# Performance work log

Measured on AMD Instinct MI355X. Metric: run time of the kernel, lower is better.

## Reference

```python
import jax, jax.numpy as jnp
import numpy as np

C = 256      # channels
G = 8        # groups
Cg = C // G  # channels per group (32, %16==0)
KS = 3       # kernel_size
PAD = 1
STRIDE = 1
DIL = 1
OS = 1.0     # offset_scale
DW = 3       # dw_kernel_size
Kg = KS * KS                      # sample points per group (remove_center=0)
D_OM = int(np.ceil(G * Kg * 3 / 8) * 8)  # 216, offset_mask linear out dim
N, H, W = 16, 56, 56


def setup_inputs() -> dict:
    key = jax.random.key(0)
    ks = jax.random.split(key, 8)
    inp = {}
    inp['ref'] = jax.random.normal(ks[0], (N, C, H, W), jnp.float32)
    inp['input'] = jax.random.normal(ks[1], (N, C, H, W), jnp.float32)
    inp['value_w'] = jax.random.normal(ks[2], (C, C), jnp.float32) * (1.0 / np.sqrt(C))
    inp['value_b'] = jnp.zeros((C,), jnp.float32)
    inp['dw_w'] = jax.random.normal(ks[3], (C, 2, DW, DW), jnp.float32) * 0.1
    inp['dw_b'] = jnp.zeros((C,), jnp.float32)
    # original zero-inits offset_mask; use small random weights so sampling is non-trivial
    inp['om_w'] = jax.random.normal(ks[4], (D_OM, C), jnp.float32) * 0.02
    inp['om_b'] = jnp.zeros((D_OM,), jnp.float32)
    inp['out_w'] = jax.random.normal(ks[5], (C, C), jnp.float32) * (1.0 / np.sqrt(C))
    inp['out_b'] = jnp.zeros((C,), jnp.float32)
    return inp


def _dcnv4(ref, inp, value_w, value_b, dw_w, dw_b, om_w, om_b, out_w, out_b):
    n, _, h, w = inp.shape
    # value projection on tokens (N, HW, C)
    tokens = inp.reshape(n, C, h * w).transpose(0, 2, 1)
    xv = (tokens @ value_w.T + value_b).reshape(n, h, w, G, Cg)
    # grouped depthwise-style conv on concat([input, ref]) -> offset/mask features
    cat = jnp.concatenate([inp, ref], axis=1)  # (N, 2C, H, W)
    dw = jax.lax.conv_general_dilated(
        cat, dw_w, (1, 1), ((DW // 2, DW // 2), (DW // 2, DW // 2)),
        dimension_numbers=('NCHW', 'OIHW', 'NCHW'), feature_group_count=C)
    dw = dw + dw_b[None, :, None, None]
    om = dw.transpose(0, 2, 3, 1) @ om_w.T + om_b            # (N,H,W,D_OM)
    om = om[..., :G * Kg * 3].reshape(n, h, w, G, Kg * 3)    # drop pad cols (none here)
    off = om[..., :2 * Kg].reshape(n, h, w, G, Kg, 2)        # (dx, dy) per point
    mask = om[..., 2 * Kg:]                                  # (N,H,W,G,Kg), DCNv4: no softmax
    # sampling locations (index coords): h*stride - pad + i*dil + os*dy
    ii, jj = jnp.meshgrid(jnp.arange(KS), jnp.arange(KS), indexing='ij')
    gy = (ii.reshape(-1) * DIL - PAD).astype(inp.dtype)      # (Kg,)
    gx = (jj.reshape(-1) * DIL - PAD).astype(inp.dtype)
    hh = (jnp.arange(h, dtype=inp.dtype) * STRIDE)[None, :, None, None, None]
    ww = (jnp.arange(w, dtype=inp.dtype) * STRIDE)[None, None, :, None, None]
    iy = hh + gy + OS * off[..., 1]                          # (N,H,W,G,Kg)
    ix = ww + gx + OS * off[..., 0]
    # bilinear sample with zero padding, mask-weighted sum over points
    y0 = jnp.floor(iy); x0 = jnp.floor(ix)
    fy = iy - y0; fx = ix - x0
    y0i = y0.astype(jnp.int32); x0i = x0.astype(jnp.int32)
    nidx = jnp.arange(n)[:, None, None, None, None]
    gidx = jnp.arange(G)[None, None, None, :, None]
    out = jnp.zeros((n, h, w, G, Cg), inp.dtype)
    for dy in (0, 1):
        for dx in (0, 1):
            yy = y0i + dy; xx = x0i + dx
            wgt = (fy if dy else 1.0 - fy) * (fx if dx else 1.0 - fx)
            valid = (yy >= 0) & (yy < h) & (xx >= 0) & (xx < w)
            yyc = jnp.clip(yy, 0, h - 1); xxc = jnp.clip(xx, 0, w - 1)
            gathered = xv[nidx, yyc, xxc, gidx]              # (N,H,W,G,Kg,Cg)
            out = out + jnp.einsum('nhwgp,nhwgpc->nhwgc', wgt * valid * mask, gathered)
    y = out.reshape(n, h * w, C) @ out_w.T + out_b
    return y.transpose(0, 2, 1).reshape(n, C, h, w)


def reference(ref, input, value_w, value_b, dw_w, dw_b, om_w, om_b, out_w, out_b):
    return _dcnv4(ref, input, value_w, value_b, dw_w, dw_b, om_w, om_b, out_w, out_b)
```

## Files before the change

kernel.cpp:

```cpp
#include <hip/hip_runtime.h>

#define HW 3136
#define WID 56
#define HEI 56
#define NCH 256
#define NB 16

typedef __attribute__((ext_vector_type(8))) short bf16x8;
typedef __attribute__((ext_vector_type(8))) unsigned short u16x8;
typedef __attribute__((ext_vector_type(4))) float f32x4;

__device__ __forceinline__ unsigned int f2bf(float f) {
    unsigned int x = __float_as_uint(f);
    return (x + 0x7fffu + ((x >> 16) & 1u)) >> 16;
}
__device__ __forceinline__ float bf2f(unsigned short u) {
    return __uint_as_float(((unsigned int)u) << 16);
}

__global__ __launch_bounds__(256) void cvt_weights(const float* __restrict__ vw,
                                                   const float* __restrict__ ow,
                                                   const float* __restrict__ outw,
                                                   unsigned short* __restrict__ dvw,
                                                   unsigned short* __restrict__ dow,
                                                   unsigned short* __restrict__ doutw) {
    int i = blockIdx.x * 256 + threadIdx.x;
    if (i < 65536) dvw[i] = (unsigned short)f2bf(vw[i]);
    else if (i < 120832) dow[i - 65536] = (unsigned short)f2bf(ow[i - 65536]);
    else if (i < 186368) doutw[i - 120832] = (unsigned short)f2bf(outw[i - 120832]);
}

template <int DOUT, int A_MODE, int OUT_MODE>
__global__ __launch_bounds__(256) void gemm_kernel(const void* __restrict__ Aptr,
                                                   const unsigned short* __restrict__ Bw,
                                                   const float* __restrict__ bias,
                                                   void* __restrict__ Out) {
    int bid = blockIdx.x;
    int nt = bid & 1;
    int mt = (bid >> 1) % 49;
    int n = (bid >> 1) / 49;
    int p0 = mt * 64;
    int tid = threadIdx.x;
    int lane = tid & 63;
    int wv = tid >> 6;
    int wm = wv & 1, wn = wv >> 1;
    int n0 = nt * 128;

    __shared__ __align__(16) char lds[8192 + 16384];
    char* As = lds;
    char* Bs = lds + 8192;

    int l15 = lane & 15;
    int l4 = lane >> 4;

    f32x4 acc[2][4];
    #pragma unroll
    for (int nf = 0; nf < 4; ++nf) {
        int ch = n0 + wn * 64 + nf * 16 + l15;
        float bv = (ch < DOUT) ? bias[ch] : 0.f;
        #pragma unroll
        for (int mf = 0; mf < 2; ++mf) acc[mf][nf] = (f32x4){bv, bv, bv, bv};
    }

    for (int t = 0; t < 4; ++t) {
        int k0 = t * 64;
        if (A_MODE == 0) {
            int px = tid & 63, kq = tid >> 6;
            const float* src = (const float*)Aptr + ((size_t)(n * 256 + k0 + kq * 16)) * HW + p0 + px;
            #pragma unroll
            for (int h = 0; h < 2; ++h) {
                u16x8 v;
                #pragma unroll
                for (int j = 0; j < 8; ++j) v[j] = (unsigned short)f2bf(src[(size_t)(h * 8 + j) * HW]);
                int byte = (px * 128 + (kq * 16 + h * 8) * 2) ^ ((px & 7) << 4);
                *(u16x8*)(As + byte) = v;
            }
        } else if (A_MODE == 1) {
            int px = tid & 63, kq = tid >> 6;
            const unsigned short* src = (const unsigned short*)Aptr + ((size_t)(n * 256 + k0 + kq * 16)) * HW + p0 + px;
            #pragma unroll
            for (int h = 0; h < 2; ++h) {
                u16x8 v;
                #pragma unroll
                for (int j = 0; j < 8; ++j) v[j] = src[(size_t)(h * 8 + j) * HW];
                int byte = (px * 128 + (kq * 16 + h * 8) * 2) ^ ((px & 7) << 4);
                *(u16x8*)(As + byte) = v;
            }
        } else {
            int row = tid >> 2, q = tid & 3;
            const unsigned short* src = (const unsigned short*)Aptr + ((size_t)(n * HW) + p0 + row) * 256 + k0 + q * 16;
            #pragma unroll
            for (int h = 0; h < 2; ++h) {
                u16x8 v = *(const u16x8*)(src + h * 8);
                int byte = (row * 128 + (q * 16 + h * 8) * 2) ^ ((row & 7) << 4);
                *(u16x8*)(As + byte) = v;
            }
        }
        {
            int bch = tid >> 1, kh = tid & 1;
            int ch = n0 + bch;
            bool valid = (ch < DOUT);
            const unsigned short* src = Bw + (size_t)ch * 256 + k0 + kh * 32;
            #pragma unroll
            for (int q = 0; q < 4; ++q) {
                u16x8 v = (u16x8){0, 0, 0, 0, 0, 0, 0, 0};
                if (valid) v = *(const u16x8*)(src + q * 8);
                int byte = (bch * 128 + (kh * 32 + q * 8) * 2) ^ ((bch & 7) << 4);
                *(u16x8*)(Bs + byte) = v;
            }
        }
        __syncthreads();
        bf16x8 af[2][2], bfr[4][2];
        #pragma unroll
        for (int mf = 0; mf < 2; ++mf)
            #pragma unroll
            for (int kf = 0; kf < 2; ++kf) {
                int row = wm * 32 + mf * 16 + l15;
                int byte = (row * 128 + (kf * 32 + l4 * 8) * 2) ^ ((row & 7) << 4);
                af[mf][kf] = *(bf16x8*)(As + byte);
            }
        #pragma unroll
        for (int nf = 0; nf < 4; ++nf)
            #pragma unroll
            for (int kf = 0; kf < 2; ++kf) {
                int row = wn * 64 + nf * 16 + l15;
                int byte = (row * 128 + (kf * 32 + l4 * 8) * 2) ^ ((row & 7) << 4);
                bfr[nf][kf] = *(bf16x8*)(Bs + byte);
            }
        #pragma unroll
        for (int mf = 0; mf < 2; ++mf)
            #pragma unroll
            for (int nf = 0; nf < 4; ++nf)
                #pragma unroll
                for (int kf = 0; kf < 2; ++kf)
                    acc[mf][nf] = __builtin_amdgcn_mfma_f32_16x16x32_bf16(af[mf][kf], bfr[nf][kf], acc[mf][nf], 0, 0, 0);
        __syncthreads();
    }

    #pragma unroll
    for (int mf = 0; mf < 2; ++mf) {
        int pxb = p0 + wm * 32 + mf * 16 + l4 * 4;
        #pragma unroll
        for (int nf = 0; nf < 4; ++nf) {
            int ch = n0 + wn * 64 + nf * 16 + l15;
            if (OUT_MODE == 0) {
                if (ch < DOUT) {
                    float* o = (float*)Out + ((size_t)n * HW + pxb) * DOUT + ch;
                    #pragma unroll
                    for (int j = 0; j < 4; ++j) o[(size_t)j * DOUT] = acc[mf][nf][j];
                }
            } else if (OUT_MODE == 1) {
                unsigned short* o = (unsigned short*)Out + ((size_t)n * HW + pxb) * 256 + ch;
                #pragma unroll
                for (int j = 0; j < 4; ++j) o[(size_t)j * 256] = (unsigned short)f2bf(acc[mf][nf][j]);
            } else {
                float* o = (float*)Out + ((size_t)(n * 256 + ch)) * HW + pxb;
                *(f32x4*)o = acc[mf][nf];
            }
        }
    }
}

__global__ __launch_bounds__(256) void dwconv_kernel(const float* __restrict__ input,
                                                     const float* __restrict__ ref,
                                                     const float* __restrict__ dw_w,
                                                     const float* __restrict__ dw_b,
                                                     unsigned short* __restrict__ out) {
    int blk = blockIdx.x;
    int yt = blk % 14;
    int cb = (blk / 14) & 63;
    int n = blk / (14 * 64);
    int tid = threadIdx.x;
    int x = tid & 63;
    int c = cb * 4 + (tid >> 6);
    int y0 = yt * 4;

    const float* src = (c < 128) ? input : ref;
    int ch0 = (c < 128) ? (2 * c) : (2 * c - 256);

    float w[18];
    #pragma unroll
    for (int i = 0; i < 18; ++i) w[i] = dw_w[c * 18 + i];

    if (x < WID) {
        float bv = dw_b[c];
        float acc[4] = {bv, bv, bv, bv};
        #pragma unroll
        for (int ch = 0; ch < 2; ++ch) {
            const float* base = src + (size_t)(n * NCH + ch0 + ch) * HW;
            #pragma unroll
            for (int r = 0; r < 6; ++r) {
                int yy = y0 - 1 + r;
                bool vy = (yy >= 0) && (yy < HEI);
                const float* row = base + yy * WID;
                float lt = (vy && x > 0) ? row[x - 1] : 0.f;
                float md = vy ? row[x] : 0.f;
                float rt = (vy && x < WID - 1) ? row[x + 1] : 0.f;
                #pragma unroll
                for (int o = 0; o < 4; ++o) {
                    int ky = r - o;
                    if (ky >= 0 && ky < 3) {
                        acc[o] += lt * w[ch * 9 + ky * 3 + 0] + md * w[ch * 9 + ky * 3 + 1] + rt * w[ch * 9 + ky * 3 + 2];
                    }
                }
            }
        }
        unsigned short* o = out + (size_t)(n * NCH + c) * HW + y0 * WID + x;
        #pragma unroll
        for (int j = 0; j < 4; ++j) o[j * WID] = (unsigned short)f2bf(acc[j]);
    }
}

__global__ __launch_bounds__(256) void sample_kernel(const unsigned short* __restrict__ xv,
                                                     const float* __restrict__ om,
                                                     unsigned short* __restrict__ sout) {
    int blk = blockIdx.x;
    int n = blk / (HW / 16);
    int p0 = (blk % (HW / 16)) * 16;
    int tid = threadIdx.x;

    __shared__ __align__(16) float swt[1152][4];
    __shared__ __align__(8) ushort soff[1152][4];

    for (int i = tid; i < 1152; i += 256) {
        int pix = i / 72;
        int r = i % 72;
        int g = r / 9;
        int pt = r % 9;
        int glob = p0 + pix;
        int py = glob / WID, px = glob % WID;
        const float* ob = om + ((size_t)n * HW + glob) * 216 + g * 27;
        float ox = ob[2 * pt];
        float oy = ob[2 * pt + 1];
        float m = ob[18 + pt];
        float iy = (float)(py + pt / 3 - 1) + oy;
        float ix = (float)(px + pt % 3 - 1) + ox;
        float fy0 = floorf(iy), fx0 = floorf(ix);
        float fy = iy - fy0, fx = ix - fx0;
        int y0 = (int)fy0, x0 = (int)fx0;
        #pragma unroll
        for (int dy = 0; dy < 2; ++dy) {
            #pragma unroll
            for (int dx = 0; dx < 2; ++dx) {
                int yy = y0 + dy, xx = x0 + dx;
                bool valid = (yy >= 0) & (yy < HEI) & (xx >= 0) & (xx < WID);
                int yc = min(max(yy, 0), HEI - 1);
                int xc = min(max(xx, 0), WID - 1);
                float wv = (dy ? fy : 1.f - fy) * (dx ? fx : 1.f - fx) * m;
                swt[i][dy * 2 + dx] = valid ? wv : 0.f;
                soff[i][dy * 2 + dx] = (ushort)(yc * WID + xc);
            }
        }
    }
    __syncthreads();

    int pix = tid >> 4;
    int t16 = tid & 15;
    const unsigned short* xvb = xv + (size_t)n * HW * 256;
    unsigned short* so = sout + ((size_t)n * HW + p0 + pix) * 256;

    #pragma unroll
    for (int i = 0; i < 2; ++i) {
        int chunk = t16 + 16 * i;
        int g = chunk >> 2, c8 = chunk & 3;
        int widx = pix * 72 + g * 9;
        const unsigned short* xc = xvb + g * 32 + c8 * 8;
        float acc[8];
        #pragma unroll
        for (int j = 0; j < 8; ++j) acc[j] = 0.f;
        #pragma unroll
        for (int pt = 0; pt < 9; ++pt) {
            float4 w = *(const float4*)&swt[widx + pt][0];
            ushort4 o = *(const ushort4*)&soff[widx + pt][0];
            u16x8 r0 = *(const u16x8*)(xc + (size_t)o.x * 256);
            u16x8 r1 = *(const u16x8*)(xc + (size_t)o.y * 256);
            u16x8 r2 = *(const u16x8*)(xc + (size_t)o.z * 256);
            u16x8 r3 = *(const u16x8*)(xc + (size_t)o.w * 256);
            #pragma unroll
            for (int j = 0; j < 8; ++j) {
                acc[j] += w.x * bf2f(r0[j]) + w.y * bf2f(r1[j]) + w.z * bf2f(r2[j]) + w.w * bf2f(r3[j]);
            }
        }
        u16x8 st;
        #pragma unroll
        for (int j = 0; j < 8; ++j) st[j] = (unsigned short)f2bf(acc[j]);
        *(u16x8*)(so + g * 32 + c8 * 8) = st;
    }
}

extern "C" void kernel_launch(void* const* d_in, const int* in_sizes, int n_in,
                              void* d_out, int out_size, void* d_ws, size_t ws_size,
                              hipStream_t stream) {
    const float* ref     = (const float*)d_in[0];
    const float* input   = (const float*)d_in[1];
    const float* value_w = (const float*)d_in[2];
    const float* value_b = (const float*)d_in[3];
    const float* dw_w    = (const float*)d_in[4];
    const float* dw_b    = (const float*)d_in[5];
    const float* om_w    = (const float*)d_in[6];
    const float* om_b    = (const float*)d_in[7];
    const float* out_w   = (const float*)d_in[8];
    const float* out_b   = (const float*)d_in[9];
    float* out = (float*)d_out;

    char* ws = (char*)d_ws;
    const size_t BF = (size_t)NB * HW * 256 * 2;
    unsigned short* xv   = (unsigned short*)(ws);
    unsigned short* dwb  = (unsigned short*)(ws + BF);
    unsigned short* sout = (unsigned short*)(ws + 2 * BF);
    float* om            = (float*)(ws + 3 * BF);
    char* wbase          = ws + 3 * BF + (size_t)NB * HW * 216 * 4;
    unsigned short* vw_bf   = (unsigned short*)(wbase);
    unsigned short* ow_bf   = (unsigned short*)(wbase + 131072);
    unsigned short* outw_bf = (unsigned short*)(wbase + 131072 + 110592);

    cvt_weights<<<728, 256, 0, stream>>>(value_w, om_w, out_w, vw_bf, ow_bf, outw_bf);
    gemm_kernel<256, 0, 1><<<NB * 49 * 2, 256, 0, stream>>>(input, vw_bf, value_b, xv);
    dwconv_kernel<<<NB * 64 * 14, 256, 0, stream>>>(input, ref, dw_w, dw_b, dwb);
    gemm_kernel<216, 1, 0><<<NB * 49 * 2, 256, 0, stream>>>(dwb, ow_bf, om_b, om);
    sample_kernel<<<NB * (HW / 16), 256, 0, stream>>>(xv, om, sout);
    gemm_kernel<256, 2, 2><<<NB * 49 * 2, 256, 0, stream>>>(sout, outw_bf, out_b, out);
}
```

Baseline: 291.8 us.

## Enlarge GEMM M-tile to 128 over flattened batch; store xv fp32, offsets bf16

Each GEMM block now covers 128 rows instead of 64, taken from the flattened N*HW pixel space so tiles may cross image boundaries. This halves the number of blocks and reuses each B tile across more rows. The value projection now writes fp32 xv, and the sampler gathers fp32 with vector FMAs instead of converting from bf16. The offset/mask GEMM now writes bf16 rather than fp32, which halves that traffic but lowers offset precision, while the fp32 xv doubles the sampler's gather bandwidth.

```diff
diff --git a/kernel.cpp b/kernel.cpp
--- a/kernel.cpp
+++ b/kernel.cpp
@@ -5,6 +5,7 @@
 #define HEI 56
 #define NCH 256
 #define NB 16
+#define MTOT (NB * HW)
 
 typedef __attribute__((ext_vector_type(8))) short bf16x8;
 typedef __attribute__((ext_vector_type(8))) unsigned short u16x8;
@@ -37,62 +38,59 @@
                                                    void* __restrict__ Out) {
     int bid = blockIdx.x;
     int nt = bid & 1;
-    int mt = (bid >> 1) % 49;
-    int n = (bid >> 1) / 49;
-    int p0 = mt * 64;
+    int mt = bid >> 1;
+    int p0 = mt * 128;
     int tid = threadIdx.x;
     int lane = tid & 63;
     int wv = tid >> 6;
     int wm = wv & 1, wn = wv >> 1;
     int n0 = nt * 128;
 
-    __shared__ __align__(16) char lds[8192 + 16384];
+    __shared__ __align__(16) char lds[16384 + 16384];
     char* As = lds;
-    char* Bs = lds + 8192;
+    char* Bs = lds + 16384;
 
     int l15 = lane & 15;
     int l4 = lane >> 4;
 
-    f32x4 acc[2][4];
+    f32x4 acc[4][4];
     #pragma unroll
     for (int nf = 0; nf < 4; ++nf) {
         int ch = n0 + wn * 64 + nf * 16 + l15;
         float bv = (ch < DOUT) ? bias[ch] : 0.f;
         #pragma unroll
-        for (int mf = 0; mf < 2; ++mf) acc[mf][nf] = (f32x4){bv, bv, bv, bv};
+        for (int mf = 0; mf < 4; ++mf) acc[mf][nf] = (f32x4){bv, bv, bv, bv};
     }
 
     for (int t = 0; t < 4; ++t) {
         int k0 = t * 64;
-        if (A_MODE == 0) {
-            int px = tid & 63, kq = tid >> 6;
-            const float* src = (const float*)Aptr + ((size_t)(n * 256 + k0 + kq * 16)) * HW + p0 + px;
-            #pragma unroll
-            for (int h = 0; h < 2; ++h) {
+        if (A_MODE == 0 || A_MODE == 1) {
+            int px = tid & 127, kh = tid >> 7;
+            unsigned int gpix = p0 + px;
+            unsigned int n = gpix / HW;
+            unsigned int rem = gpix - n * HW;
+            #pragma unroll
+            for (int h = 0; h < 4; ++h) {
                 u16x8 v;
-                #pragma unroll
-                for (int j = 0; j < 8; ++j) v[j] = (unsigned short)f2bf(src[(size_t)(h * 8 + j) * HW]);
-                int byte = (px * 128 + (kq * 16 + h * 8) * 2) ^ ((px & 7) << 4);
+                if (A_MODE == 0) {
+                    const float* src = (const float*)Aptr + ((size_t)(n * 256 + k0 + kh * 32 + h * 8)) * HW + rem;
+                    #pragma unroll
+                    for (int j = 0; j < 8; ++j) v[j] = (unsigned short)f2bf(src[(size_t)j * HW]);
+                } else {
+                    const unsigned short* src = (const unsigned short*)Aptr + ((size_t)(n * 256 + k0 + kh * 32 + h * 8)) * HW + rem;
+                    #pragma unroll
+                    for (int j = 0; j < 8; ++j) v[j] = src[(size_t)j * HW];
+                }
+                int byte = (px * 128 + (kh * 32 + h * 8) * 2) ^ ((px & 7) << 4);
                 *(u16x8*)(As + byte) = v;
             }
-        } else if (A_MODE == 1) {
-            int px = tid & 63, kq = tid >> 6;
-            const unsigned short* src = (const unsigned short*)Aptr + ((size_t)(n * 256 + k0 + kq * 16)) * HW + p0 + px;
-            #pragma unroll
-            for (int h = 0; h < 2; ++h) {
-                u16x8 v;
-                #pragma unroll
-                for (int j = 0; j < 8; ++j) v[j] = src[(size_t)(h * 8 + j) * HW];
-                int byte = (px * 128 + (kq * 16 + h * 8) * 2) ^ ((px & 7) << 4);
-                *(u16x8*)(As + byte) = v;
-            }
         } else {
-            int row = tid >> 2, q = tid & 3;
-            const unsigned short* src = (const unsigned short*)Aptr + ((size_t)(n * HW) + p0 + row) * 256 + k0 + q * 16;
-            #pragma unroll
-            for (int h = 0; h < 2; ++h) {
+            int row = tid >> 1, q = tid & 1;
+            const unsigned short* src = (const unsigned short*)Aptr + (size_t)(p0 + row) * 256 + k0 + q * 32;
+            #pragma unroll
+            for (int h = 0; h < 4; ++h) {
                 u16x8 v = *(const u16x8*)(src + h * 8);
-                int byte = (row * 128 + (q * 16 + h * 8) * 2) ^ ((row & 7) << 4);
+                int byte = (row * 128 + (q * 32 + h * 8) * 2) ^ ((row & 7) << 4);
                 *(u16x8*)(As + byte) = v;
             }
         }
@@ -110,12 +108,12 @@
             }
         }
         __syncthreads();
-        bf16x8 af[2][2], bfr[4][2];
-        #pragma unroll
-        for (int mf = 0; mf < 2; ++mf)
+        bf16x8 af[4][2], bfr[4][2];
+        #pragma unroll
+        for (int mf = 0; mf < 4; ++mf)
             #pragma unroll
             for (int kf = 0; kf < 2; ++kf) {
-                int row = wm * 32 + mf * 16 + l15;
+                int row = wm * 64 + mf * 16 + l15;
                 int byte = (row * 128 + (kf * 32 + l4 * 8) * 2) ^ ((row & 7) << 4);
                 af[mf][kf] = *(bf16x8*)(As + byte);
             }
@@ -128,7 +126,7 @@
                 bfr[nf][kf] = *(bf16x8*)(Bs + byte);
             }
         #pragma unroll
-        for (int mf = 0; mf < 2; ++mf)
+        for (int mf = 0; mf < 4; ++mf)
             #pragma unroll
             for (int nf = 0; nf < 4; ++nf)
                 #pragma unroll
@@ -138,23 +136,28 @@
     }
 
     #pragma unroll
-    for (int mf = 0; mf < 2; ++mf) {
-        int pxb = p0 + wm * 32 + mf * 16 + l4 * 4;
+    for (int mf = 0; mf < 4; ++mf) {
+        int pxb = wm * 64 + mf * 16 + l4 * 4;
+        unsigned int gpix = p0 + pxb;
         #pragma unroll
         for (int nf = 0; nf < 4; ++nf) {
             int ch = n0 + wn * 64 + nf * 16 + l15;
             if (OUT_MODE == 0) {
                 if (ch < DOUT) {
-                    float* o = (float*)Out + ((size_t)n * HW + pxb) * DOUT + ch;
+                    float* o = (float*)Out + (size_t)gpix * DOUT + ch;
                     #pragma unroll
                     for (int j = 0; j < 4; ++j) o[(size_t)j * DOUT] = acc[mf][nf][j];
                 }
             } else if (OUT_MODE == 1) {
-                unsigned short* o = (unsigned short*)Out + ((size_t)n * HW + pxb) * 256 + ch;
-                #pragma unroll
-                for (int j = 0; j < 4; ++j) o[(size_t)j * 256] = (unsigned short)f2bf(acc[mf][nf][j]);
+                if (ch < DOUT) {
+                    unsigned short* o = (unsigned short*)Out + (size_t)gpix * DOUT + ch;
+                    #pragma unroll
+                    for (int j = 0; j < 4; ++j) o[(size_t)j * DOUT] = (unsigned short)f2bf(acc[mf][nf][j]);
+                }
             } else {
-                float* o = (float*)Out + ((size_t)(n * 256 + ch)) * HW + pxb;
+                unsigned int n = gpix / HW;
+                unsigned int rem = gpix - n * HW;
+                float* o = (float*)Out + ((size_t)(n * 256 + ch)) * HW + rem;
                 *(f32x4*)o = acc[mf][nf];
             }
         }
@@ -211,8 +214,8 @@
     }
 }
 
-__global__ __launch_bounds__(256) void sample_kernel(const unsigned short* __restrict__ xv,
-                                                     const float* __restrict__ om,
+__global__ __launch_bounds__(256) void sample_kernel(const float* __restrict__ xv,
+                                                     const unsigned short* __restrict__ om,
                                                      unsigned short* __restrict__ sout) {
     int blk = blockIdx.x;
     int n = blk / (HW / 16);
@@ -229,10 +232,10 @@
         int pt = r % 9;
         int glob = p0 + pix;
         int py = glob / WID, px = glob % WID;
-        const float* ob = om + ((size_t)n * HW + glob) * 216 + g * 27;
-        float ox = ob[2 * pt];
-        float oy = ob[2 * pt + 1];
-        float m = ob[18 + pt];
+        const unsigned short* ob = om + ((size_t)n * HW + glob) * 216 + g * 27;
+        float ox = bf2f(ob[2 * pt]);
+        float oy = bf2f(ob[2 * pt + 1]);
+        float m = bf2f(ob[18 + pt]);
         float iy = (float)(py + pt / 3 - 1) + oy;
         float ix = (float)(px + pt % 3 - 1) + ox;
         float fy0 = floorf(iy), fx0 = floorf(ix);
@@ -256,7 +259,7 @@
 
     int pix = tid >> 4;
     int t16 = tid & 15;
-    const unsigned short* xvb = xv + (size_t)n * HW * 256;
+    const float* xvb = xv + (size_t)n * HW * 256;
     unsigned short* so = sout + ((size_t)n * HW + p0 + pix) * 256;
 
     #pragma unroll
@@ -264,26 +267,29 @@
         int chunk = t16 + 16 * i;
         int g = chunk >> 2, c8 = chunk & 3;
         int widx = pix * 72 + g * 9;
-        const unsigned short* xc = xvb + g * 32 + c8 * 8;
-        float acc[8];
-        #pragma unroll
-        for (int j = 0; j < 8; ++j) acc[j] = 0.f;
+        const float* xc = xvb + g * 32 + c8 * 8;
+        f32x4 a0 = (f32x4){0.f, 0.f, 0.f, 0.f};
+        f32x4 a1 = (f32x4){0.f, 0.f, 0.f, 0.f};
         #pragma unroll
         for (int pt = 0; pt < 9; ++pt) {
             float4 w = *(const float4*)&swt[widx + pt][0];
             ushort4 o = *(const ushort4*)&soff[widx + pt][0];
-            u16x8 r0 = *(const u16x8*)(xc + (size_t)o.x * 256);
-            u16x8 r1 = *(const u16x8*)(xc + (size_t)o.y * 256);
-            u16x8 r2 = *(const u16x8*)(xc + (size_t)o.z * 256);
-            u16x8 r3 = *(const u16x8*)(xc + (size_t)o.w * 256);
-            #pragma unroll
-            for (int j = 0; j < 8; ++j) {
-                acc[j] += w.x * bf2f(r0[j]) + w.y * bf2f(r1[j]) + w.z * bf2f(r2[j]) + w.w * bf2f(r3[j]);
-            }
+            const float* s0 = xc + (size_t)o.x * 256;
+            const float* s1 = xc + (size_t)o.y * 256;
+            const float* s2 = xc + (size_t)o.z * 256;
+            const float* s3 = xc + (size_t)o.w * 256;
+            f32x4 w0 = (f32x4){w.x, w.x, w.x, w.x};
+            f32x4 w1 = (f32x4){w.y, w.y, w.y, w.y};
+            f32x4 w2 = (f32x4){w.z, w.z, w.z, w.z};
+            f32x4 w3 = (f32x4){w.w, w.w, w.w, w.w};
+            a0 += w0 * *(const f32x4*)(s0) + w1 * *(const f32x4*)(s1) + w2 * *(const f32x4*)(s2) + w3 * *(const f32x4*)(s3);
+            a1 += w0 * *(const f32x4*)(s0 + 4) + w1 * *(const f32x4*)(s1 + 4) + w2 * *(const f32x4*)(s2 + 4) + w3 * *(const f32x4*)(s3 + 4);
         }
         u16x8 st;
         #pragma unroll
-        for (int j = 0; j < 8; ++j) st[j] = (unsigned short)f2bf(acc[j]);
+        for (int j = 0; j < 4; ++j) st[j] = (unsigned short)f2bf(a0[j]);
+        #pragma unroll
+        for (int j = 0; j < 4; ++j) st[4 + j] = (unsigned short)f2bf(a1[j]);
         *(u16x8*)(so + g * 32 + c8 * 8) = st;
     }
 }
@@ -304,20 +310,19 @@
     float* out = (float*)d_out;
 
     char* ws = (char*)d_ws;
-    const size_t BF = (size_t)NB * HW * 256 * 2;
-    unsigned short* xv   = (unsigned short*)(ws);
-    unsigned short* dwb  = (unsigned short*)(ws + BF);
-    unsigned short* sout = (unsigned short*)(ws + 2 * BF);
-    float* om            = (float*)(ws + 3 * BF);
-    char* wbase          = ws + 3 * BF + (size_t)NB * HW * 216 * 4;
+    float* xv            = (float*)ws;
+    unsigned short* dwb  = (unsigned short*)(ws + (size_t)MTOT * 256 * 4);
+    unsigned short* sout = (unsigned short*)(ws + (size_t)MTOT * 256 * 6);
+    unsigned short* omb  = (unsigned short*)(ws + (size_t)MTOT * 256 * 8);
+    char* wbase          = ws + (size_t)MTOT * 256 * 8 + (size_t)MTOT * 216 * 2;
     unsigned short* vw_bf   = (unsigned short*)(wbase);
     unsigned short* ow_bf   = (unsigned short*)(wbase + 131072);
     unsigned short* outw_bf = (unsigned short*)(wbase + 131072 + 110592);
 
     cvt_weights<<<728, 256, 0, stream>>>(value_w, om_w, out_w, vw_bf, ow_bf, outw_bf);
-    gemm_kernel<256, 0, 1><<<NB * 49 * 2, 256, 0, stream>>>(input, vw_bf, value_b, xv);
+    gemm_kernel<256, 0, 0><<<(MTOT / 128) * 2, 256, 0, stream>>>(input, vw_bf, value_b, xv);
     dwconv_kernel<<<NB * 64 * 14, 256, 0, stream>>>(input, ref, dw_w, dw_b, dwb);
-    gemm_kernel<216, 1, 0><<<NB * 49 * 2, 256, 0, stream>>>(dwb, ow_bf, om_b, om);
-    sample_kernel<<<NB * (HW / 16), 256, 0, stream>>>(xv, om, sout);
-    gemm_kernel<256, 2, 2><<<NB * 49 * 2, 256, 0, stream>>>(sout, outw_bf, out_b, out);
-}
+    gemm_kernel<216, 1, 1><<<(MTOT / 128) * 2, 256, 0, stream>>>(dwb, ow_bf, om_b, omb);
+    sample_kernel<<<NB * (HW / 16), 256, 0, stream>>>(xv, omb, sout);
+    gemm_kernel<256, 2, 2><<<(MTOT / 128) * 2, 256, 0, stream>>>(sout, outw_bf, out_b, out);
+}
```

New measurement: 330.7 us. 1.13x slower.
